# Performance work log

Measured on AMD Instinct MI355X. Metric: run time of the kernel, lower is better.

The kernel has to match this reference:

```python
import jax, jax.numpy as jnp
import numpy as np

ALPHA = 0.9
CAND_LEN_LIMIT = 16
DOC_LEN_LIMIT = 256
EMBED_DIM = 768
BATCH = 8


def _tri_num(n):
    return n * (n + 1) // 2


def _build_alpha_buffers(doc_len, max_cand_len, alpha):
    """Vectorized construction of the 5 FOFE context alpha buffers.

    Candidate c = (start i, span s) enumerated by start then span, matching the
    original get_contexts_alpha_buffers ordering. end e = i + s.
      buf0 candidate ctx      : alpha^(e-j) for i <= j <= e
      buf1 left ctx excl cand : alpha^(i-1-j) for j <= i-1 (zero when i == 0)
      buf2 left ctx incl cand : alpha^(e-j) for j <= e
      buf3 right ctx excl cand: alpha^(j-1-e) for j >= e+1
      buf4 right ctx incl cand: alpha^(j-i) for j >= i
    """
    starts, spans = [], []
    for i in range(doc_len):
        n = max_cand_len if i < doc_len - max_cand_len else doc_len - i
        starts += [i] * n
        spans += list(range(n))
    s = np.asarray(starts)[:, None]              # [n_cand, 1]
    e = (np.asarray(starts) + np.asarray(spans))[:, None]
    j = np.arange(doc_len)[None, :]              # [1, doc_len]

    def pw(p, m):
        return np.where(m, alpha ** np.where(m, p, 0), 0.0).astype(np.float32)

    buf0 = pw(e - j, (j >= s) & (j <= e))
    buf1 = pw(s - 1 - j, (j <= s - 1) & (s > 0))
    buf2 = pw(e - j, j <= e)
    buf3 = pw(j - 1 - e, j >= e + 1)
    buf4 = pw(j - s, j >= s)
    cands_pos = np.concatenate([s, e], axis=1).astype(np.float32)  # [n_cand, 2]
    return (buf0, buf1, buf2, buf3, buf4), cands_pos


def setup_inputs() -> dict:
    key = jax.random.key(0)
    k1, k2 = jax.random.split(key)
    x_input = jax.random.normal(k1, (BATCH, DOC_LEN_LIMIT, EMBED_DIM), dtype=jnp.float32)
    x_mask = jax.random.randint(k2, (BATCH, DOC_LEN_LIMIT), 0, 2, dtype=jnp.int32)
    return {"x_input": x_input, "x_mask": x_mask}


def reference(x_input, x_mask):
    batch = x_input.shape[0]
    doc_len = min(x_input.shape[1], DOC_LEN_LIMIT)
    max_cand_len = min(CAND_LEN_LIMIT, doc_len)
    bufs_np, cands_pos_np = _build_alpha_buffers(doc_len, max_cand_len, ALPHA)
    buf0, buf1, buf2, buf3, buf4 = [jnp.asarray(b) for b in bufs_np]
    n_cand = buf0.shape[0]

    # concat order for has_lr_ctx_cand_incl and has_lr_ctx_cand_excl both True:
    # [left_excl, left_incl, cand, right_incl, right_excl]
    all_bufs = jnp.stack([buf1, buf2, buf0, buf4, buf3], axis=0)  # [5, n_cand, L]
    # one big contraction instead of 5 bmms
    codes = jnp.einsum('kcl,bld->bkcd', all_bufs, x_input)        # [B,5,n_cand,D]
    fofe_codes = codes.transpose(0, 2, 1, 3).reshape(batch, n_cand, 5 * x_input.shape[2])

    cands_pos = jnp.broadcast_to(jnp.asarray(cands_pos_np)[None], (batch, n_cand, 2))
    padded_cands = (jnp.einsum('cl,bl->bc', buf0, x_mask.astype(jnp.float32))[..., None] > 0)
    return fofe_codes, cands_pos, padded_cands
```

## Files before the change

### kernel.cpp

```cpp
#include <hip/hip_runtime.h>

#define NB 8
#define LEN 256
#define DIM 768
#define NC 3976
#define OFF_POS 122142720
#define OFF_PAD (122142720 + 63616)

constexpr float ALPHA_F = 0.9f;
constexpr float A32 = 0.03433683820292512f;

__global__ __launch_bounds__(256) void scan_kernel(const float* __restrict__ x,
                                                   float* __restrict__ P,
                                                   float* __restrict__ S) {
    const int dl = threadIdx.x & 31;
    const int chunk = threadIdx.x >> 5;
    const int d = blockIdx.x * 32 + dl;
    const int b = blockIdx.y;
    const int dir = blockIdx.z;
    const float* __restrict__ xb = x + (size_t)b * LEN * DIM;
    float* __restrict__ ob = (dir ? S : P) + (size_t)b * LEN * DIM;

    float vals[32];
    float acc = 0.f;
#pragma unroll
    for (int t = 0; t < 32; ++t) {
        const int lm = chunk * 32 + t;
        const int l = dir ? (LEN - 1 - lm) : lm;
        acc = fmaf(ALPHA_F, acc, xb[l * DIM + d]);
        vals[t] = acc;
    }

    __shared__ float ends[8][32];
    ends[chunk][dl] = acc;
    __syncthreads();

    float carry = 0.f;
    for (int k = 0; k < chunk; ++k)
        carry = fmaf(A32, carry, ends[k][dl]);

    float w = ALPHA_F;
#pragma unroll
    for (int t = 0; t < 32; ++t) {
        const int lm = chunk * 32 + t;
        const int l = dir ? (LEN - 1 - lm) : lm;
        ob[l * DIM + d] = fmaf(w, carry, vals[t]);
        w *= ALPHA_F;
    }
}

__global__ __launch_bounds__(192) void out_kernel(const float* __restrict__ P,
                                                  const float* __restrict__ S,
                                                  const int* __restrict__ mask,
                                                  float* __restrict__ out) {
    const int c = blockIdx.x;
    const int b = blockIdx.y;
    const int t = threadIdx.x;

    int i, s;
    if (c < 3856) {
        i = c >> 4;
        s = c & 15;
    } else {
        int r = c - 3856;
        int u = 0, off = 0;
        while (off + (15 - u) <= r) { off += 15 - u; ++u; }
        i = 241 + u;
        s = r - off;
    }
    const int e = i + s;

    float w = ALPHA_F;
    for (int q = 0; q < s; ++q) w *= ALPHA_F;

    const float4 z4 = make_float4(0.f, 0.f, 0.f, 0.f);
    const float4* __restrict__ Pb = (const float4*)(P + (size_t)b * LEN * DIM);
    const float4* __restrict__ Sb = (const float4*)(S + (size_t)b * LEN * DIM);

    const float4 pm1 = (i > 0) ? Pb[(i - 1) * 192 + t] : z4;
    const float4 pe = Pb[e * 192 + t];
    const float4 si = Sb[i * 192 + t];
    const float4 se1 = (e < LEN - 1) ? Sb[(e + 1) * 192 + t] : z4;
    float4 cand;
    cand.x = fmaf(-w, pm1.x, pe.x);
    cand.y = fmaf(-w, pm1.y, pe.y);
    cand.z = fmaf(-w, pm1.z, pe.z);
    cand.w = fmaf(-w, pm1.w, pe.w);

    float4* __restrict__ o = (float4*)out + (size_t)(b * NC + c) * 960;
    o[0 * 192 + t] = pm1;
    o[1 * 192 + t] = pe;
    o[2 * 192 + t] = cand;
    o[3 * 192 + t] = si;
    o[4 * 192 + t] = se1;

    if (t < 64) {
        int m = 0;
        if (t < 16 && t <= s) m = mask[b * LEN + i + t];
        unsigned long long ball = __ballot(m != 0);
        if (t == 0) {
            out[OFF_POS + (size_t)(b * NC + c) * 2] = (float)i;
            out[OFF_POS + (size_t)(b * NC + c) * 2 + 1] = (float)e;
            out[OFF_PAD + (size_t)(b * NC + c)] = ball ? 1.f : 0.f;
        }
    }
}

extern "C" void kernel_launch(void* const* d_in, const int* in_sizes, int n_in,
                              void* d_out, int out_size, void* d_ws, size_t ws_size,
                              hipStream_t stream) {
    const float* x = (const float*)d_in[0];
    const int* mask = (const int*)d_in[1];
    float* out = (float*)d_out;
    float* P = (float*)d_ws;
    float* S = P + (size_t)NB * LEN * DIM;

    scan_kernel<<<dim3(DIM / 32, NB, 2), 256, 0, stream>>>(x, P, S);
    out_kernel<<<dim3(NC, NB), 192, 0, stream>>>(P, S, mask, out);
}
```

Measured before the change: 109.8 us.

## Process all spans of a start position per block with nontemporal stores

The output kernel now launches one block per (batch, start) pair instead of per candidate, and loops over up to 16 spans. This reuses the P[i-1] and S[i] loads across spans, removes the per-candidate index decoding, and replaces the power loop with a running multiply. Output stores become nontemporal to avoid polluting cache with the large write-once result, and the position/padding outputs are computed with a single ballot prefix mask. Fewer blocks (2048) each do more serial work, which may reduce memory-level parallelism per block.

```diff
diff --git a/kernel.cpp b/kernel.cpp
--- a/kernel.cpp
+++ b/kernel.cpp
@@ -9,6 +9,8 @@
 
 constexpr float ALPHA_F = 0.9f;
 constexpr float A32 = 0.03433683820292512f;
+
+typedef float f4 __attribute__((ext_vector_type(4)));
 
 __global__ __launch_bounds__(256) void scan_kernel(const float* __restrict__ x,
                                                    float* __restrict__ P,
@@ -53,55 +55,52 @@
                                                   const float* __restrict__ S,
                                                   const int* __restrict__ mask,
                                                   float* __restrict__ out) {
-    const int c = blockIdx.x;
-    const int b = blockIdx.y;
+    const int b = blockIdx.x;
+    const int i = blockIdx.y;
     const int t = threadIdx.x;
 
-    int i, s;
-    if (c < 3856) {
-        i = c >> 4;
-        s = c & 15;
+    int n, c0;
+    if (i <= 240) {
+        n = 16;
+        c0 = i * 16;
     } else {
-        int r = c - 3856;
-        int u = 0, off = 0;
-        while (off + (15 - u) <= r) { off += 15 - u; ++u; }
-        i = 241 + u;
-        s = r - off;
+        const int r = LEN - i;
+        n = r;
+        c0 = 3856 + 120 - r * (r + 1) / 2;
     }
-    const int e = i + s;
 
+    const f4 z4 = (f4)0.f;
+    const f4* __restrict__ Pb = (const f4*)(P + (size_t)b * LEN * DIM);
+    const f4* __restrict__ Sb = (const f4*)(S + (size_t)b * LEN * DIM);
+
+    const f4 pm1 = (i > 0) ? Pb[(i - 1) * 192 + t] : z4;
+    const f4 si = Sb[i * 192 + t];
+
+    f4* o = (f4*)out + (size_t)(b * NC + c0) * 960 + t;
     float w = ALPHA_F;
-    for (int q = 0; q < s; ++q) w *= ALPHA_F;
+    for (int s = 0; s < n; ++s) {
+        const int e = i + s;
+        const f4 pe = Pb[e * 192 + t];
+        const f4 se1 = (e < LEN - 1) ? Sb[(e + 1) * 192 + t] : z4;
+        const f4 cand = pe - w * pm1;
 
-    const float4 z4 = make_float4(0.f, 0.f, 0.f, 0.f);
-    const float4* __restrict__ Pb = (const float4*)(P + (size_t)b * LEN * DIM);
-    const float4* __restrict__ Sb = (const float4*)(S + (size_t)b * LEN * DIM);
-
-    const float4 pm1 = (i > 0) ? Pb[(i - 1) * 192 + t] : z4;
-    const float4 pe = Pb[e * 192 + t];
-    const float4 si = Sb[i * 192 + t];
-    const float4 se1 = (e < LEN - 1) ? Sb[(e + 1) * 192 + t] : z4;
-    float4 cand;
-    cand.x = fmaf(-w, pm1.x, pe.x);
-    cand.y = fmaf(-w, pm1.y, pe.y);
-    cand.z = fmaf(-w, pm1.z, pe.z);
-    cand.w = fmaf(-w, pm1.w, pe.w);
-
-    float4* __restrict__ o = (float4*)out + (size_t)(b * NC + c) * 960;
-    o[0 * 192 + t] = pm1;
-    o[1 * 192 + t] = pe;
-    o[2 * 192 + t] = cand;
-    o[3 * 192 + t] = si;
-    o[4 * 192 + t] = se1;
+        __builtin_nontemporal_store(pm1, o + 0 * 192);
+        __builtin_nontemporal_store(pe, o + 1 * 192);
+        __builtin_nontemporal_store(cand, o + 2 * 192);
+        __builtin_nontemporal_store(si, o + 3 * 192);
+        __builtin_nontemporal_store(se1, o + 4 * 192);
+        o += 960;
+        w *= ALPHA_F;
+    }
 
     if (t < 64) {
-        int m = 0;
-        if (t < 16 && t <= s) m = mask[b * LEN + i + t];
-        unsigned long long ball = __ballot(m != 0);
-        if (t == 0) {
-            out[OFF_POS + (size_t)(b * NC + c) * 2] = (float)i;
-            out[OFF_POS + (size_t)(b * NC + c) * 2 + 1] = (float)e;
-            out[OFF_PAD + (size_t)(b * NC + c)] = ball ? 1.f : 0.f;
+        const int m = (t < n) ? mask[b * LEN + i + t] : 0;
+        const unsigned long long ball = __ballot(m != 0);
+        if (t < n) {
+            const size_t c = (size_t)(b * NC + c0 + t);
+            out[OFF_POS + c * 2] = (float)i;
+            out[OFF_POS + c * 2 + 1] = (float)(i + t);
+            out[OFF_PAD + c] = (ball & ((2ull << t) - 1)) ? 1.f : 0.f;
         }
     }
 }
@@ -116,5 +115,5 @@
     float* S = P + (size_t)NB * LEN * DIM;
 
     scan_kernel<<<dim3(DIM / 32, NB, 2), 256, 0, stream>>>(x, P, S);
-    out_kernel<<<dim3(NC, NB), 192, 0, stream>>>(P, S, mask, out);
+    out_kernel<<<dim3(NB, LEN), 192, 0, stream>>>(P, S, mask, out);
 }
```

New measurement: 110.3 us. No clear change (+0.5%).
